# Optimization experiments

Hardware: AMD Instinct MI355X
Metric: run time of the kernel (lower is better)

The kernel has to match this reference:

```python
import jax, jax.numpy as jnp
import numpy as np

N0, N1, N2 = 80000, 40000, 20000
E1, E2 = 500000, 250000
FIN = 128        # in_channels
H = 2            # heads
C1 = 64          # hidden_channels -> layer1 out per head (concat -> 128)
C2 = 64          # out_channels -> layer2 out per head (mean over heads)
ED = 10          # edge_dim per embedding, total edge feat = 2*ED = 20
NTYPE, NTS = 23, 1158


def setup_inputs() -> dict:
    key = jax.random.key(0)
    ks = jax.random.split(key, 48)
    sc = 0.05
    inp = {
        "x": jax.random.normal(ks[0], (N0, FIN), jnp.float32),
        "ei1_src": jax.random.randint(ks[1], (E1,), 0, N0),
        "ei1_dst": jax.random.randint(ks[2], (E1,), 0, N1),
        "et1": jax.random.randint(ks[3], (E1,), 0, NTYPE),
        "ets1": jax.random.randint(ks[4], (E1,), 0, NTS),
        "ei2_src": jax.random.randint(ks[5], (E2,), 0, N1),
        "ei2_dst": jax.random.randint(ks[6], (E2,), 0, N2),
        "et2": jax.random.randint(ks[7], (E2,), 0, NTYPE),
        "ets2": jax.random.randint(ks[8], (E2,), 0, NTS),
        # shared edge embeddings (Linear(23,10), Linear(1158,10))
        "edge_W": jax.random.normal(ks[9], (ED, NTYPE), jnp.float32) * sc,
        "edge_b": jax.random.normal(ks[10], (ED,), jnp.float32) * sc,
        "time_W": jax.random.normal(ks[11], (ED, NTS), jnp.float32) * sc,
        "time_b": jax.random.normal(ks[12], (ED,), jnp.float32) * sc,
    }
    # layer 1: in=128, heads=2, C=64, concat=True (out dim 128)
    hc1 = H * C1
    inp["Wq1"] = jax.random.normal(ks[13], (hc1, FIN), jnp.float32) * sc
    inp["bq1"] = jnp.zeros((hc1,), jnp.float32)
    inp["Wk1"] = jax.random.normal(ks[14], (hc1, FIN), jnp.float32) * sc
    inp["bk1"] = jnp.zeros((hc1,), jnp.float32)
    inp["Wv1"] = jax.random.normal(ks[15], (hc1, FIN), jnp.float32) * sc
    inp["bv1"] = jnp.zeros((hc1,), jnp.float32)
    inp["We1"] = jax.random.normal(ks[16], (hc1, 2 * ED), jnp.float32) * sc
    inp["Wskip1"] = jax.random.normal(ks[17], (hc1, FIN), jnp.float32) * sc
    inp["bskip1"] = jnp.zeros((hc1,), jnp.float32)
    inp["Wbeta1"] = jax.random.normal(ks[18], (1, 3 * hc1), jnp.float32) * sc
    inp["ln_g"] = jnp.ones((hc1,), jnp.float32)
    inp["ln_b"] = jnp.zeros((hc1,), jnp.float32)
    # layer 2: in=128, heads=2, C=64, concat=False (out dim 64)
    hc2 = H * C2
    inp["Wq2"] = jax.random.normal(ks[19], (hc2, hc1), jnp.float32) * sc
    inp["bq2"] = jnp.zeros((hc2,), jnp.float32)
    inp["Wk2"] = jax.random.normal(ks[20], (hc2, hc1), jnp.float32) * sc
    inp["bk2"] = jnp.zeros((hc2,), jnp.float32)
    inp["Wv2"] = jax.random.normal(ks[21], (hc2, hc1), jnp.float32) * sc
    inp["bv2"] = jnp.zeros((hc2,), jnp.float32)
    inp["We2"] = jax.random.normal(ks[22], (hc2, 2 * ED), jnp.float32) * sc
    inp["Wskip2"] = jax.random.normal(ks[23], (C2, hc1), jnp.float32) * sc
    inp["bskip2"] = jnp.zeros((C2,), jnp.float32)
    inp["Wbeta2"] = jax.random.normal(ks[24], (1, 3 * C2), jnp.float32) * sc
    return inp


def _edge_feat(et, ets, edge_W, edge_b, time_W, time_b):
    # one_hot(e) @ W.T + b == W.T[e] + b (avoids materializing huge one-hot)
    return jnp.concatenate([jnp.take(edge_W.T, et, axis=0) + edge_b,
                            jnp.take(time_W.T, ets, axis=0) + time_b], axis=-1)


def _conv(x_src, x_dst, src, dst, ef, Wq, bq, Wk, bk, Wv, bv, We,
          Wskip, bskip, Wbeta, concat):
    n_dst = x_dst.shape[0]
    HC = Wq.shape[0]
    C = HC // H
    q = (x_dst @ Wq.T + bq).reshape(n_dst, H, C)            # [Nd,H,C]
    k = (x_src @ Wk.T + bk)[src].reshape(-1, H, C)          # [E,H,C]
    v = (x_src @ Wv.T + bv)[src].reshape(-1, H, C)
    e = (ef @ We.T).reshape(-1, H, C)
    k = k + e
    alpha = jnp.einsum('ehc,ehc->eh', q[dst], k) / np.sqrt(C).astype(np.float32)
    # segment softmax over destination nodes
    m = jax.ops.segment_max(alpha, dst, num_segments=n_dst)
    ex = jnp.exp(alpha - m[dst])
    s = jax.ops.segment_sum(ex, dst, num_segments=n_dst)
    a = ex / (s[dst] + 1e-16)                               # [E,H]
    msg = (v + e) * a[..., None]                            # [E,H,C]
    out = jax.ops.segment_sum(msg.reshape(-1, HC), dst, num_segments=n_dst)
    out = out if concat else out.reshape(n_dst, H, C).mean(axis=1)
    x_r = x_dst @ Wskip.T + bskip
    beta = jax.nn.sigmoid(
        jnp.concatenate([out, x_r, out - x_r], axis=-1) @ Wbeta.T)  # [Nd,1]
    return beta * x_r + (1.0 - beta) * out


def _layernorm(x, g, b):
    mu = x.mean(-1, keepdims=True)
    var = x.var(-1, keepdims=True)
    return (x - mu) / jnp.sqrt(var + 1e-5) * g + b


def reference(x, ei1_src, ei1_dst, et1, ets1, ei2_src, ei2_dst, et2, ets2,
              edge_W, edge_b, time_W, time_b,
              Wq1, bq1, Wk1, bk1, Wv1, bv1, We1, Wskip1, bskip1, Wbeta1,
              ln_g, ln_b,
              Wq2, bq2, Wk2, bk2, Wv2, bv2, We2, Wskip2, bskip2, Wbeta2):
    ef1 = _edge_feat(et1, ets1, edge_W, edge_b, time_W, time_b)
    h = _conv(x, x[:N1], ei1_src, ei1_dst, ef1,
              Wq1, bq1, Wk1, bk1, Wv1, bv1, We1, Wskip1, bskip1, Wbeta1,
              concat=True)
    h = jax.nn.gelu(_layernorm(h, ln_g, ln_b), approximate=False)
    ef2 = _edge_feat(et2, ets2, edge_W, edge_b, time_W, time_b)
    o = _conv(h, h[:N2], ei2_src, ei2_dst, ef2,
              Wq2, bq2, Wk2, bk2, Wv2, bv2, We2, Wskip2, bskip2, Wbeta2,
              concat=False)
    return jax.nn.log_softmax(o, axis=-1)
```

## Files before the change

### kernel.cpp

```cpp
#include <hip/hip_runtime.h>
#include <math.h>

#define N0 80000
#define N1 40000
#define N2 20000
#define E1C 500000
#define E2C 250000
#define NTYPE 23
#define NTS 1158

#define NB1 157
#define NB2 79
#define KV1B 1250
#define QR1B 625
#define CNTB 2930
#define KV2B 625
#define QR2B 313
#define FILLB 2930

#define OFF_XB    0u
#define OFF_QR1   5120000u
#define OFF_KV1   15360000u
#define OFF_H     25600000u
#define OFF_QR2   28160000u
#define OFF_KV2   32000000u
#define OFF_WB1   37120000u
#define OFF_BP1   37160000u
#define OFF_WB2   37170000u
#define OFF_BP2   37200000u
#define OFF_TA1   37210000u
#define OFF_TB1   37213000u
#define OFF_TA2   37370000u
#define OFF_TB2   37373000u
#define OFF_RP1   37530000u
#define OFF_CUR1  37580000u
#define OFF_ED1   37630000u
#define OFF_BS1   38640000u
#define OFF_RP2   38650000u
#define OFF_CUR2  38680000u
#define OFF_ED2   38710000u
#define OFF_BS2   39220000u
#define OFF_DONE  39230000u

typedef __bf16 bf16x8 __attribute__((ext_vector_type(8)));
typedef float f32x4 __attribute__((ext_vector_type(4)));

static __device__ __forceinline__ float b2f(unsigned short u) {
    union { unsigned int i; float f; } c;
    c.i = ((unsigned int)u) << 16;
    return c.f;
}
static __device__ __forceinline__ unsigned short f2b(float f) {
    unsigned int u = __float_as_uint(f);
    unsigned int r = (u + 0x7fffu + ((u >> 16) & 1u)) >> 16;
    return (unsigned short)r;
}
static __device__ __forceinline__ bf16x8 ldfrag(const unsigned short* p) {
    return *reinterpret_cast<const bf16x8*>(p);
}

template <int CTRL>
static __device__ __forceinline__ float dpp_addstep(float v) {
    int x = __builtin_amdgcn_mov_dpp(__float_as_int(v), CTRL, 0xF, 0xF, true);
    return v + __int_as_float(x);
}
static __device__ __forceinline__ float red16(float v) {
    v = dpp_addstep<0xB1>(v);
    v = dpp_addstep<0x4E>(v);
    v = dpp_addstep<0x141>(v);
    v = dpp_addstep<0x140>(v);
    return v;
}
template <int CTRL>
static __device__ __forceinline__ float dpp_maxstep(float v) {
    int x = __builtin_amdgcn_mov_dpp(__float_as_int(v), CTRL, 0xF, 0xF, true);
    return fmaxf(v, __int_as_float(x));
}
static __device__ __forceinline__ float red16max(float v) {
    v = dpp_maxstep<0xB1>(v);
    v = dpp_maxstep<0x4E>(v);
    v = dpp_maxstep<0x141>(v);
    v = dpp_maxstep<0x140>(v);
    return v;
}

#define LDSS 136

template <int NTILES>
static __device__ __forceinline__ void dev_gemm_bf16out(
    const unsigned short* __restrict__ XB, const unsigned short* __restrict__ WB,
    const float* __restrict__ BP, unsigned short* __restrict__ Y, int n, int blk,
    unsigned short* sb) {
    constexpr int COLS = NTILES * 16;
    constexpr int HALF = NTILES / 2;
    constexpr int HCOLS = HALF * 16;
    int wave = threadIdx.x >> 6, lane = threadIdx.x & 63;
    int m = lane & 15, quad = lane >> 4;
    int rowbase = blk * 64 + wave * 16;
    int arow = rowbase + m; if (arow >= n) arow = n - 1;
    unsigned short* swave = sb + wave * 16 * LDSS;
    const unsigned short* xrow = XB + (size_t)arow * 128 + quad * 8;
    bf16x8 a0 = ldfrag(xrow), a1 = ldfrag(xrow + 32);
    bf16x8 a2 = ldfrag(xrow + 64), a3 = ldfrag(xrow + 96);
    f32x4 acc[NTILES];
#pragma unroll
    for (int t = 0; t < NTILES; t++) acc[t] = (f32x4){0.f, 0.f, 0.f, 0.f};
#pragma unroll
    for (int t = 0; t < NTILES; t++) {
        const unsigned short* wt = WB + (size_t)t * 2048 + lane * 8;
        acc[t] = __builtin_amdgcn_mfma_f32_16x16x32_bf16(a0, ldfrag(wt), acc[t], 0, 0, 0);
        acc[t] = __builtin_amdgcn_mfma_f32_16x16x32_bf16(a1, ldfrag(wt + 512), acc[t], 0, 0, 0);
        acc[t] = __builtin_amdgcn_mfma_f32_16x16x32_bf16(a2, ldfrag(wt + 1024), acc[t], 0, 0, 0);
        acc[t] = __builtin_amdgcn_mfma_f32_16x16x32_bf16(a3, ldfrag(wt + 1536), acc[t], 0, 0, 0);
    }
    int tswz_bit = (quad >> 1) & 1;
#pragma unroll
    for (int half = 0; half < 2; half++) {
#pragma unroll
        for (int t = 0; t < HALF; t++) {
            int tt = half * HALF + t;
            int tsw = t ^ tswz_bit;
            float b = BP[tt * 16 + m];
#pragma unroll
            for (int r = 0; r < 4; r++)
                swave[(quad * 4 + r) * LDSS + tsw * 16 + m] = f2b(acc[tt][r] + b);
        }
#pragma unroll
        for (int i = 0; i < 4; i++) {
            int idx = i * 64 + lane;
            int r = idx / (HCOLS / 8), g = idx % (HCOLS / 8);
            int gs = g ^ (((r >> 3) & 1) << 1);
            int grow = rowbase + r;
            if (grow < n) {
                uint4 v = *(const uint4*)&swave[r * LDSS + gs * 8];
                *(uint4*)(Y + (size_t)grow * COLS + half * HCOLS + g * 8) = v;
            }
        }
    }
}

template <int NTILES>
static __device__ __forceinline__ void dev_gemm_f32out(
    const unsigned short* __restrict__ XB, const unsigned short* __restrict__ WB,
    const float* __restrict__ BP, float* __restrict__ Y, int n, int blk) {
    constexpr int COLS = NTILES * 16;
    int wave = threadIdx.x >> 6, lane = threadIdx.x & 63;
    int m = lane & 15, quad = lane >> 4;
    int rowbase = blk * 64 + wave * 16;
    int arow = rowbase + m; if (arow >= n) arow = n - 1;
    const unsigned short* xrow = XB + (size_t)arow * 128 + quad * 8;
    bf16x8 a0 = ldfrag(xrow), a1 = ldfrag(xrow + 32);
    bf16x8 a2 = ldfrag(xrow + 64), a3 = ldfrag(xrow + 96);
    f32x4 acc[NTILES];
#pragma unroll
    for (int t = 0; t < NTILES; t++) acc[t] = (f32x4){0.f, 0.f, 0.f, 0.f};
#pragma unroll
    for (int t = 0; t < NTILES; t++) {
        const unsigned short* wt = WB + (size_t)t * 2048 + lane * 8;
        acc[t] = __builtin_amdgcn_mfma_f32_16x16x32_bf16(a0, ldfrag(wt), acc[t], 0, 0, 0);
        acc[t] = __builtin_amdgcn_mfma_f32_16x16x32_bf16(a1, ldfrag(wt + 512), acc[t], 0, 0, 0);
        acc[t] = __builtin_amdgcn_mfma_f32_16x16x32_bf16(a2, ldfrag(wt + 1024), acc[t], 0, 0, 0);
        acc[t] = __builtin_amdgcn_mfma_f32_16x16x32_bf16(a3, ldfrag(wt + 1536), acc[t], 0, 0, 0);
    }
#pragma unroll
    for (int t = 0; t < NTILES; t++) {
        float b = BP[t * 16 + m];
#pragma unroll
        for (int r = 0; r < 4; r++) {
            int grow = rowbase + quad * 4 + r;
            if (grow < n) Y[(size_t)grow * COLS + t * 16 + m] = acc[t][r] + b;
        }
    }
}

__global__ __launch_bounds__(256) void prep(
    const float* __restrict__ x, unsigned short* __restrict__ XB,
    const float* __restrict__ Wk1, const float* __restrict__ Wv1,
    const float* __restrict__ Wq1, const float* __restrict__ Wskip1,
    const float* __restrict__ bk1, const float* __restrict__ bv1,
    const float* __restrict__ bq1, const float* __restrict__ bskip1,
    const float* __restrict__ Wk2, const float* __restrict__ Wv2,
    const float* __restrict__ Wq2, const float* __restrict__ Wskip2,
    const float* __restrict__ bk2, const float* __restrict__ bv2,
    const float* __restrict__ bq2, const float* __restrict__ bskip2,
    unsigned short* __restrict__ WB1, float* __restrict__ BP1,
    unsigned short* __restrict__ WB2, float* __restrict__ BP2,
    const float* __restrict__ edge_W, const float* __restrict__ edge_b,
    const float* __restrict__ time_W, const float* __restrict__ time_b,
    const float* __restrict__ We1, const float* __restrict__ We2,
    float* __restrict__ TA1, float* __restrict__ TB1,
    float* __restrict__ TA2, float* __restrict__ TB2,
    int* __restrict__ cnt1, int* __restrict__ cnt2, int* __restrict__ done) {
    int tid = blockIdx.x * blockDim.x + threadIdx.x;
    int stride = gridDim.x * blockDim.x;
    for (int i = tid; i < N0 * 32; i += stride) {
        float4 v = *(const float4*)(x + (size_t)i * 4);
        ushort4 u;
        u.x = f2b(v.x); u.y = f2b(v.y); u.z = f2b(v.z); u.w = f2b(v.w);
        *(ushort4*)(XB + (size_t)i * 4) = u;
    }
    for (int i = tid; i < 512 * 128; i += stride) {
        int j = i & 7, l = (i >> 3) & 63, ks = (i >> 9) & 3, t = i >> 11;
        int row = t * 16 + (l & 15);
        int col = ks * 32 + ((l >> 4) & 3) * 8 + j;
        const float* w; int off;
        if (row < 128) { w = Wk1; off = 0; }
        else if (row < 256) { w = Wv1; off = 128; }
        else if (row < 384) { w = Wq1; off = 256; }
        else { w = Wskip1; off = 384; }
        WB1[i] = f2b(w[(size_t)(row - off) * 128 + col]);
    }
    for (int i = tid; i < 512; i += stride) {
        const float* b; int off;
        if (i < 128) { b = bk1; off = 0; }
        else if (i < 256) { b = bv1; off = 128; }
        else if (i < 384) { b = bq1; off = 256; }
        else { b = bskip1; off = 384; }
        BP1[i] = b[i - off];
    }
    for (int i = tid; i < 448 * 128; i += stride) {
        int j = i & 7, l = (i >> 3) & 63, ks = (i >> 9) & 3, t = i >> 11;
        int row = t * 16 + (l & 15);
        int col = ks * 32 + ((l >> 4) & 3) * 8 + j;
        const float* w; int off;
        if (row < 128) { w = Wk2; off = 0; }
        else if (row < 256) { w = Wv2; off = 128; }
        else if (row < 384) { w = Wq2; off = 256; }
        else { w = Wskip2; off = 384; }
        WB2[i] = f2b(w[(size_t)(row - off) * 128 + col]);
    }
    for (int i = tid; i < 448; i += stride) {
        const float* b; int off;
        if (i < 128) { b = bk2; off = 0; }
        else if (i < 256) { b = bv2; off = 128; }
        else if (i < 384) { b = bq2; off = 256; }
        else { b = bskip2; off = 384; }
        BP2[i] = b[i - off];
    }
    const int TBL = (NTYPE + NTS) * 128;
    for (int i = tid; i < TBL; i += stride) {
        if (i < NTYPE * 128) {
            int e = i >> 7, c = i & 127;
            float s1 = 0.f, s2 = 0.f;
#pragma unroll
            for (int j = 0; j < 10; j++) {
                float fj = edge_W[j * NTYPE + e] + edge_b[j];
                s1 += fj * We1[c * 20 + j];
                s2 += fj * We2[c * 20 + j];
            }
            TA1[i] = s1; TA2[i] = s2;
        } else {
            int u = i - NTYPE * 128;
            int ts = u >> 7, c = u & 127;
            float s1 = 0.f, s2 = 0.f;
#pragma unroll
            for (int j = 0; j < 10; j++) {
                float fj = time_W[j * NTS + ts] + time_b[j];
                s1 += fj * We1[c * 20 + 10 + j];
                s2 += fj * We2[c * 20 + 10 + j];
            }
            TB1[u] = s1; TB2[u] = s2;
        }
    }
    for (int i = tid; i < N1 + N2 + 2; i += stride) {
        if (i < N1) cnt1[i] = 0;
        else if (i < N1 + N2) cnt2[i - N1] = 0;
        else done[i - N1 - N2] = 0;
    }
}

__global__ __launch_bounds__(256) void mega_l1(
    const unsigned short* __restrict__ XB,
    const unsigned short* __restrict__ WB1, const float* __restrict__ BP1,
    unsigned short* __restrict__ KV1, float* __restrict__ QR1,
    const int* __restrict__ d1, const int* __restrict__ d2,
    int* __restrict__ cnt1, int* __restrict__ cnt2) {
    __shared__ unsigned short sbuf[4 * 16 * LDSS];
    int b = blockIdx.x;
    if (b < KV1B) {
        dev_gemm_bf16out<16>(XB, WB1, BP1, KV1, N0, b, sbuf);
    } else if (b < KV1B + QR1B) {
        dev_gemm_f32out<16>(XB, WB1 + 256 * 128, BP1 + 256, QR1, N1, b - KV1B);
    } else {
        int t = (b - KV1B - QR1B) * 256 + threadIdx.x;
        if (t < E1C) atomicAdd(&cnt1[d1[t]], 1);
        else {
            t -= E1C;
            if (t < E2C) atomicAdd(&cnt2[d2[t]], 1);
        }
    }
}

__global__ __launch_bounds__(256) void gemm_l2(
    const unsigned short* __restrict__ H,
    const unsigned short* __restrict__ WB2, const float* __restrict__ BP2,
    unsigned short* __restrict__ KV2, float* __restrict__ QR2) {
    __shared__ unsigned short sbuf[4 * 16 * LDSS];
    int b = blockIdx.x;
    if (b < KV2B) dev_gemm_bf16out<16>(H, WB2, BP2, KV2, N1, b, sbuf);
    else dev_gemm_f32out<12>(H, WB2 + 256 * 128, BP2 + 256, QR2, N2, b - KV2B);
}

__global__ __launch_bounds__(256) void csr_scan(
    int* __restrict__ cnt1, int* __restrict__ bs1, int* __restrict__ rp1,
    int* __restrict__ cnt2, int* __restrict__ bs2, int* __restrict__ rp2,
    int* __restrict__ done) {
    __shared__ int s[256];
    __shared__ int amlast;
    int b = blockIdx.x;
    int* cnt; int* bs; int* rp; int n, lb;
    if (b < NB1) { cnt = cnt1; bs = bs1; rp = rp1; n = N1; lb = b; }
    else { cnt = cnt2; bs = bs2; rp = rp2; n = N2; lb = b - NB1; }
    int t = lb * 256 + threadIdx.x;
    int v = (t < n) ? cnt[t] : 0;
    s[threadIdx.x] = v;
    __syncthreads();
    for (int off = 128; off; off >>= 1) {
        if (threadIdx.x < off) s[threadIdx.x] += s[threadIdx.x + off];
        __syncthreads();
    }
    if (threadIdx.x == 0) {
        atomicExch(&bs[lb], s[0]);
        __threadfence();
        int prev = atomicAdd(&done[0], 1);
        amlast = (prev == NB1 + NB2 - 1) ? 1 : 0;
    }
    __syncthreads();
    if (amlast) {
        int tt = threadIdx.x;
        int v1 = (tt < NB1) ? atomicAdd(&bs1[tt], 0) : 0;
        s[tt] = v1;
        __syncthreads();
        for (int off = 1; off < 256; off <<= 1) {
            int u = (tt >= off) ? s[tt - off] : 0;
            __syncthreads();
            s[tt] += u;
            __syncthreads();
        }
        if (tt < NB1) atomicExch(&bs1[tt], s[tt] - v1);
        __syncthreads();
        int v2 = (tt < NB2) ? atomicAdd(&bs2[tt], 0) : 0;
        s[tt] = v2;
        __syncthreads();
        for (int off = 1; off < 256; off <<= 1) {
            int u = (tt >= off) ? s[tt - off] : 0;
            __syncthreads();
            s[tt] += u;
            __syncthreads();
        }
        if (tt < NB2) atomicExch(&bs2[tt], s[tt] - v2);
        __threadfence();
        __syncthreads();
        if (tt == 0) atomicExch(&done[1], 1);
    }
    if (threadIdx.x == 0) {
        while (atomicAdd(&done[1], 0) == 0) __builtin_amdgcn_s_sleep(1);
    }
    __syncthreads();
    __threadfence();
    int base = atomicAdd(&bs[lb], 0);
    s[threadIdx.x] = v;
    __syncthreads();
    for (int off = 1; off < 256; off <<= 1) {
        int u = (threadIdx.x >= off) ? s[threadIdx.x - off] : 0;
        __syncthreads();
        s[threadIdx.x] += u;
        __syncthreads();
    }
    int incl = s[threadIdx.x];
    if (t < n) { rp[t] = base + incl - v; cnt[t] = 0; }
    if (t == n - 1) rp[n] = base + incl;
}

__global__ __launch_bounds__(256) void fill_both(
    const int* __restrict__ d1, const int* __restrict__ s1,
    const int* __restrict__ et1, const int* __restrict__ ets1,
    const int* __restrict__ rp1, int* __restrict__ cur1, uint2* __restrict__ ed1,
    const int* __restrict__ d2, const int* __restrict__ s2,
    const int* __restrict__ et2, const int* __restrict__ ets2,
    const int* __restrict__ rp2, int* __restrict__ cur2, uint2* __restrict__ ed2) {
    int t = blockIdx.x * 256 + threadIdx.x;
    if (t < E1C) {
        int d = d1[t];
        int pos = rp1[d] + atomicAdd(&cur1[d], 1);
        ed1[pos] = make_uint2((unsigned)s1[t],
                              (unsigned)(et1[t] | (ets1[t] << 16)));
    } else {
        t -= E1C;
        if (t < E2C) {
            int d = d2[t];
            int pos = rp2[d] + atomicAdd(&cur2[d], 1);
            ed2[pos] = make_uint2((unsigned)s2[t],
                                  (unsigned)(et2[t] | (ets2[t] << 16)));
        }
    }
}

__global__ __launch_bounds__(256) void agg_layer1(
    const int* __restrict__ rowptr, const uint2* __restrict__ ED,
    const float* __restrict__ TA, const float* __restrict__ TB,
    const float* __restrict__ QR, const unsigned short* __restrict__ KV,
    const float* __restrict__ Wbeta,
    const float* __restrict__ ln_g, const float* __restrict__ ln_b,
    unsigned short* __restrict__ hout, int n) {
    int wid = (blockIdx.x * blockDim.x + threadIdx.x) >> 6;
    int lane = threadIdx.x & 63;
    if (wid >= n) return;
    int s = lane >> 5, cg = lane & 15;
    int co = ((lane >> 4) & 1) * 64 + 4 * cg;
    int beg = rowptr[wid], end = rowptr[wid + 1];
    float4 q4 = *(const float4*)(QR + (size_t)wid * 256 + co);
    float ax = 0.f, ay = 0.f, az = 0.f, aw = 0.f, suma = 0.f;
    int p = beg + s;
    if (p < end) {
        uint2 d0 = ED[p];
        int p1 = p + 2;
        bool m1 = p1 < end;
        uint2 dn = ED[m1 ? p1 : beg];
        int sn0 = (int)d0.x, t0 = (int)(d0.y & 0xFFFF), ts0 = (int)(d0.y >> 16);
        float4 ta0 = *(const float4*)(TA + t0 * 128 + co);
        float4 tb0 = *(const float4*)(TB + ts0 * 128 + co);
        const unsigned short* kv0 = KV + (size_t)sn0 * 256;
        ushort4 ku0 = *(const ushort4*)(kv0 + co);
        ushort4 vu0 = *(const ushort4*)(kv0 + 128 + co);
        for (;;) {
            int p2 = p1 + 2;
            bool m2 = p2 < end;
            uint2 dnn = ED[m2 ? p2 : beg];
            int sn1 = (int)dn.x, t1 = (int)(dn.y & 0xFFFF), ts1 = (int)(dn.y >> 16);
            float4 ta1 = *(const float4*)(TA + t1 * 128 + co);
            float4 tb1 = *(const float4*)(TB + ts1 * 128 + co);
            const unsigned short* kv1 = KV + (size_t)sn1 * 256;
            ushort4 ku1 = *(const ushort4*)(kv1 + co);
            ushort4 vu1 = *(const ushort4*)(kv1 + 128 + co);
            float e0c = ta0.x + tb0.x, e1c = ta0.y + tb0.y;
            float e2c = ta0.z + tb0.z, e3c = ta0.w + tb0.w;
            float pp = q4.x * (b2f(ku0.x) + e0c) + q4.y * (b2f(ku0.y) + e1c)
                     + q4.z * (b2f(ku0.z) + e2c) + q4.w * (b2f(ku0.w) + e3c);
            pp = red16(pp);
            float a = __expf(pp * 0.125f);
            ax += a * (b2f(vu0.x) + e0c); ay += a * (b2f(vu0.y) + e1c);
            az += a * (b2f(vu0.z) + e2c); aw += a * (b2f(vu0.w) + e3c);
            suma += a;
            if (!m1) break;
            p1 = p2; m1 = m2; dn = dnn;
            ta0 = ta1; tb0 = tb1; ku0 = ku1; vu0 = vu1;
        }
    }
    ax += __shfl_xor(ax, 32); ay += __shfl_xor(ay, 32);
    az += __shfl_xor(az, 32); aw += __shfl_xor(aw, 32);
    suma += __shfl_xor(suma, 32);
    float inv_s = 1.f / (suma + 1e-16f);
    float ox = ax * inv_s, oy = ay * inv_s, oz = az * inv_s, ow = aw * inv_s;
    float4 r4 = *(const float4*)(QR + (size_t)wid * 256 + 128 + co);
    float4 wo = *(const float4*)(Wbeta + co);
    float4 wr = *(const float4*)(Wbeta + 128 + co);
    float4 wd = *(const float4*)(Wbeta + 256 + co);
    float pb = wo.x * ox + wr.x * r4.x + wd.x * (ox - r4.x)
             + wo.y * oy + wr.y * r4.y + wd.y * (oy - r4.y)
             + wo.z * oz + wr.z * r4.z + wd.z * (oz - r4.z)
             + wo.w * ow + wr.w * r4.w + wd.w * (ow - r4.w);
    pb = red16(pb);
    pb += __shfl_xor(pb, 16);
    float beta = 1.f / (1.f + __expf(-pb));
    float gx = beta * r4.x + (1.f - beta) * ox;
    float gy = beta * r4.y + (1.f - beta) * oy;
    float gz = beta * r4.z + (1.f - beta) * oz;
    float gw = beta * r4.w + (1.f - beta) * ow;
    float sm = gx + gy + gz + gw;
    float sq = gx * gx + gy * gy + gz * gz + gw * gw;
    sm = red16(sm); sm += __shfl_xor(sm, 16);
    sq = red16(sq); sq += __shfl_xor(sq, 16);
    float mu = sm * (1.f / 128.f);
    float var = sq * (1.f / 128.f) - mu * mu;
    float inv = rsqrtf(var + 1e-5f);
    float4 lg = *(const float4*)(ln_g + co);
    float4 lb = *(const float4*)(ln_b + co);
    float yx = (gx - mu) * inv * lg.x + lb.x;
    float yy = (gy - mu) * inv * lg.y + lb.y;
    float yz = (gz - mu) * inv * lg.z + lb.z;
    float yw = (gw - mu) * inv * lg.w + lb.w;
    const float ISQ2 = 0.70710678118654752f;
    yx = 0.5f * yx * (1.f + erff(yx * ISQ2));
    yy = 0.5f * yy * (1.f + erff(yy * ISQ2));
    yz = 0.5f * yz * (1.f + erff(yz * ISQ2));
    yw = 0.5f * yw * (1.f + erff(yw * ISQ2));
    if (s == 0) {
        ushort4 hv;
        hv.x = f2b(yx); hv.y = f2b(yy); hv.z = f2b(yz); hv.w = f2b(yw);
        *(ushort4*)(hout + (size_t)wid * 128 + co) = hv;
    }
}

__global__ __launch_bounds__(256) void agg_layer2(
    const int* __restrict__ rowptr, const uint2* __restrict__ ED,
    const float* __restrict__ TA, const float* __restrict__ TB,
    const float* __restrict__ QR, const unsigned short* __restrict__ KV,
    const float* __restrict__ Wbeta,
    float* __restrict__ o, int n) {
    int wid = (blockIdx.x * blockDim.x + threadIdx.x) >> 6;
    int lane = threadIdx.x & 63;
    if (wid >= n) return;
    int s = lane >> 5, cg = lane & 15;
    int co = ((lane >> 4) & 1) * 64 + 4 * cg;
    int beg = rowptr[wid], end = rowptr[wid + 1];
    float4 q4 = *(const float4*)(QR + (size_t)wid * 192 + co);
    float ax = 0.f, ay = 0.f, az = 0.f, aw = 0.f, suma = 0.f;
    int p = beg + s;
    if (p < end) {
        uint2 d0 = ED[p];
        int p1 = p + 2;
        bool m1 = p1 < end;
        uint2 dn = ED[m1 ? p1 : beg];
        int sn0 = (int)d0.x, t0 = (int)(d0.y & 0xFFFF), ts0 = (int)(d0.y >> 16);
        float4 ta0 = *(const float4*)(TA + t0 * 128 + co);
        float4 tb0 = *(const float4*)(TB + ts0 * 128 + co);
        const unsigned short* kv0 = KV + (size_t)sn0 * 256;
        ushort4 ku0 = *(const ushort4*)(kv0 + co);
        ushort4 vu0 = *(const ushort4*)(kv0 + 128 + co);
        for (;;) {
            int p2 = p1 + 2;
            bool m2 = p2 < end;
            uint2 dnn = ED[m2 ? p2 : beg];
            int sn1 = (int)dn.x, t1 = (int)(dn.y & 0xFFFF), ts1 = (int)(dn.y >> 16);
            float4 ta1 = *(const float4*)(TA + t1 * 128 + co);
            float4 tb1 = *(const float4*)(TB + ts1 * 128 + co);
            const unsigned short* kv1 = KV + (size_t)sn1 * 256;
            ushort4 ku1 = *(const ushort4*)(kv1 + co);
            ushort4 vu1 = *(const ushort4*)(kv1 + 128 + co);
            float e0c = ta0.x + tb0.x, e1c = ta0.y + tb0.y;
            float e2c = ta0.z + tb0.z, e3c = ta0.w + tb0.w;
            float pp = q4.x * (b2f(ku0.x) + e0c) + q4.y * (b2f(ku0.y) + e1c)
                     + q4.z * (b2f(ku0.z) + e2c) + q4.w * (b2f(ku0.w) + e3c);
            pp = red16(pp);
            float a = __expf(pp * 0.125f);
            ax += a * (b2f(vu0.x) + e0c); ay += a * (b2f(vu0.y) + e1c);
            az += a * (b2f(vu0.z) + e2c); aw += a * (b2f(vu0.w) + e3c);
            suma += a;
            if (!m1) break;
            p1 = p2; m1 = m2; dn = dnn;
            ta0 = ta1; tb0 = tb1; ku0 = ku1; vu0 = vu1;
        }
    }
    ax += __shfl_xor(ax, 32); ay += __shfl_xor(ay, 32);
    az += __shfl_xor(az, 32); aw += __shfl_xor(aw, 32);
    suma += __shfl_xor(suma, 32);
    float inv_s = 1.f / (suma + 1e-16f);
    float ox = ax * inv_s, oy = ay * inv_s, oz = az * inv_s, ow = aw * inv_s;
    ox = 0.5f * (ox + __shfl_xor(ox, 16));
    oy = 0.5f * (oy + __shfl_xor(oy, 16));
    oz = 0.5f * (oz + __shfl_xor(oz, 16));
    ow = 0.5f * (ow + __shfl_xor(ow, 16));
    float4 r4 = *(const float4*)(QR + (size_t)wid * 192 + 128 + 4 * cg);
    float4 wo = *(const float4*)(Wbeta + 4 * cg);
    float4 wr = *(const float4*)(Wbeta + 64 + 4 * cg);
    float4 wd = *(const float4*)(Wbeta + 128 + 4 * cg);
    float pb = wo.x * ox + wr.x * r4.x + wd.x * (ox - r4.x)
             + wo.y * oy + wr.y * r4.y + wd.y * (oy - r4.y)
             + wo.z * oz + wr.z * r4.z + wd.z * (oz - r4.z)
             + wo.w * ow + wr.w * r4.w + wd.w * (ow - r4.w);
    pb = red16(pb);
    float beta = 1.f / (1.f + __expf(-pb));
    float vx = beta * r4.x + (1.f - beta) * ox;
    float vy = beta * r4.y + (1.f - beta) * oy;
    float vz = beta * r4.z + (1.f - beta) * oz;
    float vw = beta * r4.w + (1.f - beta) * ow;
    float m = fmaxf(fmaxf(vx, vy), fmaxf(vz, vw));
    m = red16max(m);
    float se = __expf(vx - m) + __expf(vy - m) + __expf(vz - m) + __expf(vw - m);
    se = red16(se);
    float lse = m + logf(se);
    if (lane < 16)
        *(float4*)(o + (size_t)wid * 64 + 4 * cg) =
            make_float4(vx - lse, vy - lse, vz - lse, vw - lse);
}

extern "C" void kernel_launch(void* const* d_in, const int* in_sizes, int n_in,
                              void* d_out, int out_size, void* d_ws, size_t ws_size,
                              hipStream_t stream) {
    const float* x        = (const float*)d_in[0];
    const int*   ei1_src  = (const int*)d_in[1];
    const int*   ei1_dst  = (const int*)d_in[2];
    const int*   et1      = (const int*)d_in[3];
    const int*   ets1     = (const int*)d_in[4];
    const int*   ei2_src  = (const int*)d_in[5];
    const int*   ei2_dst  = (const int*)d_in[6];
    const int*   et2      = (const int*)d_in[7];
    const int*   ets2     = (const int*)d_in[8];
    const float* edge_W   = (const float*)d_in[9];
    const float* edge_b   = (const float*)d_in[10];
    const float* time_W   = (const float*)d_in[11];
    const float* time_b   = (const float*)d_in[12];
    const float* Wq1      = (const float*)d_in[13];
    const float* bq1      = (const float*)d_in[14];
    const float* Wk1      = (const float*)d_in[15];
    const float* bk1      = (const float*)d_in[16];
    const float* Wv1      = (const float*)d_in[17];
    const float* bv1      = (const float*)d_in[18];
    const float* We1      = (const float*)d_in[19];
    const float* Wskip1   = (const float*)d_in[20];
    const float* bskip1   = (const float*)d_in[21];
    const float* Wbeta1   = (const float*)d_in[22];
    const float* ln_g     = (const float*)d_in[23];
    const float* ln_b     = (const float*)d_in[24];
    const float* Wq2      = (const float*)d_in[25];
    const float* bq2      = (const float*)d_in[26];
    const float* Wk2      = (const float*)d_in[27];
    const float* bk2      = (const float*)d_in[28];
    const float* Wv2      = (const float*)d_in[29];
    const float* bv2      = (const float*)d_in[30];
    const float* We2      = (const float*)d_in[31];
    const float* Wskip2   = (const float*)d_in[32];
    const float* bskip2   = (const float*)d_in[33];
    const float* Wbeta2   = (const float*)d_in[34];

    float* ws = (float*)d_ws;
    unsigned short* xb  = (unsigned short*)(ws + OFF_XB);
    float* qr1          = ws + OFF_QR1;
    unsigned short* kv1 = (unsigned short*)(ws + OFF_KV1);
    unsigned short* h   = (unsigned short*)(ws + OFF_H);
    float* qr2          = ws + OFF_QR2;
    unsigned short* kv2 = (unsigned short*)(ws + OFF_KV2);
    unsigned short* wb1 = (unsigned short*)(ws + OFF_WB1);
    float* bp1          = ws + OFF_BP1;
    unsigned short* wb2 = (unsigned short*)(ws + OFF_WB2);
    float* bp2          = ws + OFF_BP2;
    float* ta1          = ws + OFF_TA1;
    float* tb1          = ws + OFF_TB1;
    float* ta2          = ws + OFF_TA2;
    float* tb2          = ws + OFF_TB2;
    int*   rp1          = (int*)(ws + OFF_RP1);
    int*   cur1         = (int*)(ws + OFF_CUR1);
    uint2* ed1          = (uint2*)(ws + OFF_ED1);
    int*   bs1          = (int*)(ws + OFF_BS1);
    int*   rp2          = (int*)(ws + OFF_RP2);
    int*   cur2         = (int*)(ws + OFF_CUR2);
    uint2* ed2          = (uint2*)(ws + OFF_ED2);
    int*   bs2          = (int*)(ws + OFF_BS2);
    int*   done         = (int*)(ws + OFF_DONE);

    prep<<<2048, 256, 0, stream>>>(
        x, xb,
        Wk1, Wv1, Wq1, Wskip1, bk1, bv1, bq1, bskip1,
        Wk2, Wv2, Wq2, Wskip2, bk2, bv2, bq2, bskip2,
        wb1, bp1, wb2, bp2,
        edge_W, edge_b, time_W, time_b, We1, We2,
        ta1, tb1, ta2, tb2, cur1, cur2, done);
    mega_l1<<<KV1B + QR1B + CNTB, 256, 0, stream>>>(
        xb, wb1, bp1, kv1, qr1, ei1_dst, ei2_dst, cur1, cur2);
    csr_scan<<<NB1 + NB2, 256, 0, stream>>>(cur1, bs1, rp1, cur2, bs2, rp2, done);
    fill_both<<<FILLB, 256, 0, stream>>>(
        ei1_dst, ei1_src, et1, ets1, rp1, cur1, ed1,
        ei2_dst, ei2_src, et2, ets2, rp2, cur2, ed2);
    agg_layer1<<<(N1 + 3) / 4, 256, 0, stream>>>(rp1, ed1,
        ta1, tb1, qr1, kv1, Wbeta1, ln_g, ln_b, h, N1);
    gemm_l2<<<KV2B + QR2B, 256, 0, stream>>>(h, wb2, bp2, kv2, qr2);
    agg_layer2<<<(N2 + 3) / 4, 256, 0, stream>>>(rp2, ed2,
        ta2, tb2, qr2, kv2, Wbeta2, (float*)d_out, N2);
}
```

Before: 392.4 us.

## Use persistent atomic-ticket scheduling and deeper prefetch in aggregation kernels

Both aggregation kernels become persistent. Each wave grabs batches of four destination nodes from a global atomic ticket counter instead of being assigned one node per wave, and the grid shrinks to a fixed block count. The edge loop now prefetches two edges ahead instead of one, to hide more gather latency. The atomic ticket balances the uneven per-node degree, at the cost of atomic contention and more live registers.

```diff
diff --git a/kernel.cpp b/kernel.cpp
--- a/kernel.cpp
+++ b/kernel.cpp
@@ -262,7 +262,7 @@
             TB1[u] = s1; TB2[u] = s2;
         }
     }
-    for (int i = tid; i < N1 + N2 + 2; i += stride) {
+    for (int i = tid; i < N1 + N2 + 4; i += stride) {
         if (i < N1) cnt1[i] = 0;
         else if (i < N1 + N2) cnt2[i - N1] = 0;
         else done[i - N1 - N2] = 0;
@@ -402,93 +402,108 @@
     const float* __restrict__ QR, const unsigned short* __restrict__ KV,
     const float* __restrict__ Wbeta,
     const float* __restrict__ ln_g, const float* __restrict__ ln_b,
-    unsigned short* __restrict__ hout, int n) {
-    int wid = (blockIdx.x * blockDim.x + threadIdx.x) >> 6;
+    unsigned short* __restrict__ hout, int n, int* __restrict__ ticket) {
     int lane = threadIdx.x & 63;
-    if (wid >= n) return;
     int s = lane >> 5, cg = lane & 15;
     int co = ((lane >> 4) & 1) * 64 + 4 * cg;
-    int beg = rowptr[wid], end = rowptr[wid + 1];
-    float4 q4 = *(const float4*)(QR + (size_t)wid * 256 + co);
-    float ax = 0.f, ay = 0.f, az = 0.f, aw = 0.f, suma = 0.f;
-    int p = beg + s;
-    if (p < end) {
-        uint2 d0 = ED[p];
-        int p1 = p + 2;
-        bool m1 = p1 < end;
-        uint2 dn = ED[m1 ? p1 : beg];
-        int sn0 = (int)d0.x, t0 = (int)(d0.y & 0xFFFF), ts0 = (int)(d0.y >> 16);
-        float4 ta0 = *(const float4*)(TA + t0 * 128 + co);
-        float4 tb0 = *(const float4*)(TB + ts0 * 128 + co);
-        const unsigned short* kv0 = KV + (size_t)sn0 * 256;
-        ushort4 ku0 = *(const ushort4*)(kv0 + co);
-        ushort4 vu0 = *(const ushort4*)(kv0 + 128 + co);
-        for (;;) {
-            int p2 = p1 + 2;
-            bool m2 = p2 < end;
-            uint2 dnn = ED[m2 ? p2 : beg];
-            int sn1 = (int)dn.x, t1 = (int)(dn.y & 0xFFFF), ts1 = (int)(dn.y >> 16);
-            float4 ta1 = *(const float4*)(TA + t1 * 128 + co);
-            float4 tb1 = *(const float4*)(TB + ts1 * 128 + co);
-            const unsigned short* kv1 = KV + (size_t)sn1 * 256;
-            ushort4 ku1 = *(const ushort4*)(kv1 + co);
-            ushort4 vu1 = *(const ushort4*)(kv1 + 128 + co);
-            float e0c = ta0.x + tb0.x, e1c = ta0.y + tb0.y;
-            float e2c = ta0.z + tb0.z, e3c = ta0.w + tb0.w;
-            float pp = q4.x * (b2f(ku0.x) + e0c) + q4.y * (b2f(ku0.y) + e1c)
-                     + q4.z * (b2f(ku0.z) + e2c) + q4.w * (b2f(ku0.w) + e3c);
-            pp = red16(pp);
-            float a = __expf(pp * 0.125f);
-            ax += a * (b2f(vu0.x) + e0c); ay += a * (b2f(vu0.y) + e1c);
-            az += a * (b2f(vu0.z) + e2c); aw += a * (b2f(vu0.w) + e3c);
-            suma += a;
-            if (!m1) break;
-            p1 = p2; m1 = m2; dn = dnn;
-            ta0 = ta1; tb0 = tb1; ku0 = ku1; vu0 = vu1;
-        }
-    }
-    ax += __shfl_xor(ax, 32); ay += __shfl_xor(ay, 32);
-    az += __shfl_xor(az, 32); aw += __shfl_xor(aw, 32);
-    suma += __shfl_xor(suma, 32);
-    float inv_s = 1.f / (suma + 1e-16f);
-    float ox = ax * inv_s, oy = ay * inv_s, oz = az * inv_s, ow = aw * inv_s;
-    float4 r4 = *(const float4*)(QR + (size_t)wid * 256 + 128 + co);
-    float4 wo = *(const float4*)(Wbeta + co);
-    float4 wr = *(const float4*)(Wbeta + 128 + co);
-    float4 wd = *(const float4*)(Wbeta + 256 + co);
-    float pb = wo.x * ox + wr.x * r4.x + wd.x * (ox - r4.x)
-             + wo.y * oy + wr.y * r4.y + wd.y * (oy - r4.y)
-             + wo.z * oz + wr.z * r4.z + wd.z * (oz - r4.z)
-             + wo.w * ow + wr.w * r4.w + wd.w * (ow - r4.w);
-    pb = red16(pb);
-    pb += __shfl_xor(pb, 16);
-    float beta = 1.f / (1.f + __expf(-pb));
-    float gx = beta * r4.x + (1.f - beta) * ox;
-    float gy = beta * r4.y + (1.f - beta) * oy;
-    float gz = beta * r4.z + (1.f - beta) * oz;
-    float gw = beta * r4.w + (1.f - beta) * ow;
-    float sm = gx + gy + gz + gw;
-    float sq = gx * gx + gy * gy + gz * gz + gw * gw;
-    sm = red16(sm); sm += __shfl_xor(sm, 16);
-    sq = red16(sq); sq += __shfl_xor(sq, 16);
-    float mu = sm * (1.f / 128.f);
-    float var = sq * (1.f / 128.f) - mu * mu;
-    float inv = rsqrtf(var + 1e-5f);
-    float4 lg = *(const float4*)(ln_g + co);
-    float4 lb = *(const float4*)(ln_b + co);
-    float yx = (gx - mu) * inv * lg.x + lb.x;
-    float yy = (gy - mu) * inv * lg.y + lb.y;
-    float yz = (gz - mu) * inv * lg.z + lb.z;
-    float yw = (gw - mu) * inv * lg.w + lb.w;
-    const float ISQ2 = 0.70710678118654752f;
-    yx = 0.5f * yx * (1.f + erff(yx * ISQ2));
-    yy = 0.5f * yy * (1.f + erff(yy * ISQ2));
-    yz = 0.5f * yz * (1.f + erff(yz * ISQ2));
-    yw = 0.5f * yw * (1.f + erff(yw * ISQ2));
-    if (s == 0) {
-        ushort4 hv;
-        hv.x = f2b(yx); hv.y = f2b(yy); hv.z = f2b(yz); hv.w = f2b(yw);
-        *(ushort4*)(hout + (size_t)wid * 128 + co) = hv;
+    for (;;) {
+        int base0 = 0;
+        if (lane == 0) base0 = atomicAdd(ticket, 4);
+        int nb = __shfl(base0, 0);
+        if (nb >= n) return;
+        int lim = nb + 4 < n ? nb + 4 : n;
+        for (int wid = nb; wid < lim; wid++) {
+            int beg = rowptr[wid], end = rowptr[wid + 1];
+            float4 q4 = *(const float4*)(QR + (size_t)wid * 256 + co);
+            float ax = 0.f, ay = 0.f, az = 0.f, aw = 0.f, suma = 0.f;
+            int p = beg + s;
+            if (p < end) {
+                uint2 d0 = ED[p];
+                int pA = p + 2;  bool mA = pA < end;
+                uint2 d1 = ED[mA ? pA : beg];
+                int pB = p + 4;  bool mB = pB < end;
+                uint2 d2 = ED[mB ? pB : beg];
+                int sn0 = (int)d0.x, t0 = (int)(d0.y & 0xFFFF), ts0 = (int)(d0.y >> 16);
+                float4 ta0 = *(const float4*)(TA + t0 * 128 + co);
+                float4 tb0 = *(const float4*)(TB + ts0 * 128 + co);
+                const unsigned short* kv0 = KV + (size_t)sn0 * 256;
+                ushort4 ku0 = *(const ushort4*)(kv0 + co);
+                ushort4 vu0 = *(const ushort4*)(kv0 + 128 + co);
+                int sn1 = (int)d1.x, t1 = (int)(d1.y & 0xFFFF), ts1 = (int)(d1.y >> 16);
+                float4 ta1 = *(const float4*)(TA + t1 * 128 + co);
+                float4 tb1 = *(const float4*)(TB + ts1 * 128 + co);
+                const unsigned short* kv1 = KV + (size_t)sn1 * 256;
+                ushort4 ku1 = *(const ushort4*)(kv1 + co);
+                ushort4 vu1 = *(const ushort4*)(kv1 + 128 + co);
+                for (;;) {
+                    int pC = pB + 2; bool mC = pC < end;
+                    uint2 d3 = ED[mC ? pC : beg];
+                    int sn2 = (int)d2.x, t2 = (int)(d2.y & 0xFFFF), ts2 = (int)(d2.y >> 16);
+                    float4 ta2 = *(const float4*)(TA + t2 * 128 + co);
+                    float4 tb2 = *(const float4*)(TB + ts2 * 128 + co);
+                    const unsigned short* kv2 = KV + (size_t)sn2 * 256;
+                    ushort4 ku2 = *(const ushort4*)(kv2 + co);
+                    ushort4 vu2 = *(const ushort4*)(kv2 + 128 + co);
+                    float e0c = ta0.x + tb0.x, e1c = ta0.y + tb0.y;
+                    float e2c = ta0.z + tb0.z, e3c = ta0.w + tb0.w;
+                    float pp = q4.x * (b2f(ku0.x) + e0c) + q4.y * (b2f(ku0.y) + e1c)
+                             + q4.z * (b2f(ku0.z) + e2c) + q4.w * (b2f(ku0.w) + e3c);
+                    pp = red16(pp);
+                    float a = __expf(pp * 0.125f);
+                    ax += a * (b2f(vu0.x) + e0c); ay += a * (b2f(vu0.y) + e1c);
+                    az += a * (b2f(vu0.z) + e2c); aw += a * (b2f(vu0.w) + e3c);
+                    suma += a;
+                    if (!mA) break;
+                    ta0 = ta1; tb0 = tb1; ku0 = ku1; vu0 = vu1;
+                    ta1 = ta2; tb1 = tb2; ku1 = ku2; vu1 = vu2;
+                    d2 = d3;
+                    mA = mB; mB = mC; pB = pC;
+                }
+            }
+            ax += __shfl_xor(ax, 32); ay += __shfl_xor(ay, 32);
+            az += __shfl_xor(az, 32); aw += __shfl_xor(aw, 32);
+            suma += __shfl_xor(suma, 32);
+            float inv_s = 1.f / (suma + 1e-16f);
+            float ox = ax * inv_s, oy = ay * inv_s, oz = az * inv_s, ow = aw * inv_s;
+            float4 r4 = *(const float4*)(QR + (size_t)wid * 256 + 128 + co);
+            float4 wo = *(const float4*)(Wbeta + co);
+            float4 wr = *(const float4*)(Wbeta + 128 + co);
+            float4 wd = *(const float4*)(Wbeta + 256 + co);
+            float pb = wo.x * ox + wr.x * r4.x + wd.x * (ox - r4.x)
+                     + wo.y * oy + wr.y * r4.y + wd.y * (oy - r4.y)
+                     + wo.z * oz + wr.z * r4.z + wd.z * (oz - r4.z)
+                     + wo.w * ow + wr.w * r4.w + wd.w * (ow - r4.w);
+            pb = red16(pb);
+            pb += __shfl_xor(pb, 16);
+            float beta = 1.f / (1.f + __expf(-pb));
+            float gx = beta * r4.x + (1.f - beta) * ox;
+            float gy = beta * r4.y + (1.f - beta) * oy;
+            float gz = beta * r4.z + (1.f - beta) * oz;
+            float gw = beta * r4.w + (1.f - beta) * ow;
+            float sm = gx + gy + gz + gw;
+            float sq = gx * gx + gy * gy + gz * gz + gw * gw;
+            sm = red16(sm); sm += __shfl_xor(sm, 16);
+            sq = red16(sq); sq += __shfl_xor(sq, 16);
+            float mu = sm * (1.f / 128.f);
+            float var = sq * (1.f / 128.f) - mu * mu;
+            float inv = rsqrtf(var + 1e-5f);
+            float4 lg = *(const float4*)(ln_g + co);
+            float4 lb = *(const float4*)(ln_b + co);
+            float yx = (gx - mu) * inv * lg.x + lb.x;
+            float yy = (gy - mu) * inv * lg.y + lb.y;
+            float yz = (gz - mu) * inv * lg.z + lb.z;
+            float yw = (gw - mu) * inv * lg.w + lb.w;
+            const float ISQ2 = 0.70710678118654752f;
+            yx = 0.5f * yx * (1.f + erff(yx * ISQ2));
+            yy = 0.5f * yy * (1.f + erff(yy * ISQ2));
+            yz = 0.5f * yz * (1.f + erff(yz * ISQ2));
+            yw = 0.5f * yw * (1.f + erff(yw * ISQ2));
+            if (s == 0) {
+                ushort4 hv;
+                hv.x = f2b(yx); hv.y = f2b(yy); hv.z = f2b(yz); hv.w = f2b(yw);
+                *(ushort4*)(hout + (size_t)wid * 128 + co) = hv;
+            }
+        }
     }
 }
 
@@ -497,82 +512,97 @@
     const float* __restrict__ TA, const float* __restrict__ TB,
     const float* __restrict__ QR, const unsigned short* __restrict__ KV,
     const float* __restrict__ Wbeta,
-    float* __restrict__ o, int n) {
-    int wid = (blockIdx.x * blockDim.x + threadIdx.x) >> 6;
+    float* __restrict__ o, int n, int* __restrict__ ticket) {
     int lane = threadIdx.x & 63;
-    if (wid >= n) return;
     int s = lane >> 5, cg = lane & 15;
     int co = ((lane >> 4) & 1) * 64 + 4 * cg;
-    int beg = rowptr[wid], end = rowptr[wid + 1];
-    float4 q4 = *(const float4*)(QR + (size_t)wid * 192 + co);
-    float ax = 0.f, ay = 0.f, az = 0.f, aw = 0.f, suma = 0.f;
-    int p = beg + s;
-    if (p < end) {
-        uint2 d0 = ED[p];
-        int p1 = p + 2;
-        bool m1 = p1 < end;
-        uint2 dn = ED[m1 ? p1 : beg];
-        int sn0 = (int)d0.x, t0 = (int)(d0.y & 0xFFFF), ts0 = (int)(d0.y >> 16);
-        float4 ta0 = *(const float4*)(TA + t0 * 128 + co);
-        float4 tb0 = *(const float4*)(TB + ts0 * 128 + co);
-        const unsigned short* kv0 = KV + (size_t)sn0 * 256;
-        ushort4 ku0 = *(const ushort4*)(kv0 + co);
-        ushort4 vu0 = *(const ushort4*)(kv0 + 128 + co);
-        for (;;) {
-            int p2 = p1 + 2;
-            bool m2 = p2 < end;
-            uint2 dnn = ED[m2 ? p2 : beg];
-            int sn1 = (int)dn.x, t1 = (int)(dn.y & 0xFFFF), ts1 = (int)(dn.y >> 16);
-            float4 ta1 = *(const float4*)(TA + t1 * 128 + co);
-            float4 tb1 = *(const float4*)(TB + ts1 * 128 + co);
-            const unsigned short* kv1 = KV + (size_t)sn1 * 256;
-            ushort4 ku1 = *(const ushort4*)(kv1 + co);
-            ushort4 vu1 = *(const ushort4*)(kv1 + 128 + co);
-            float e0c = ta0.x + tb0.x, e1c = ta0.y + tb0.y;
-            float e2c = ta0.z + tb0.z, e3c = ta0.w + tb0.w;
-            float pp = q4.x * (b2f(ku0.x) + e0c) + q4.y * (b2f(ku0.y) + e1c)
-                     + q4.z * (b2f(ku0.z) + e2c) + q4.w * (b2f(ku0.w) + e3c);
-            pp = red16(pp);
-            float a = __expf(pp * 0.125f);
-            ax += a * (b2f(vu0.x) + e0c); ay += a * (b2f(vu0.y) + e1c);
-            az += a * (b2f(vu0.z) + e2c); aw += a * (b2f(vu0.w) + e3c);
-            suma += a;
-            if (!m1) break;
-            p1 = p2; m1 = m2; dn = dnn;
-            ta0 = ta1; tb0 = tb1; ku0 = ku1; vu0 = vu1;
-        }
-    }
-    ax += __shfl_xor(ax, 32); ay += __shfl_xor(ay, 32);
-    az += __shfl_xor(az, 32); aw += __shfl_xor(aw, 32);
-    suma += __shfl_xor(suma, 32);
-    float inv_s = 1.f / (suma + 1e-16f);
-    float ox = ax * inv_s, oy = ay * inv_s, oz = az * inv_s, ow = aw * inv_s;
-    ox = 0.5f * (ox + __shfl_xor(ox, 16));
-    oy = 0.5f * (oy + __shfl_xor(oy, 16));
-    oz = 0.5f * (oz + __shfl_xor(oz, 16));
-    ow = 0.5f * (ow + __shfl_xor(ow, 16));
-    float4 r4 = *(const float4*)(QR + (size_t)wid * 192 + 128 + 4 * cg);
-    float4 wo = *(const float4*)(Wbeta + 4 * cg);
-    float4 wr = *(const float4*)(Wbeta + 64 + 4 * cg);
-    float4 wd = *(const float4*)(Wbeta + 128 + 4 * cg);
-    float pb = wo.x * ox + wr.x * r4.x + wd.x * (ox - r4.x)
-             + wo.y * oy + wr.y * r4.y + wd.y * (oy - r4.y)
-             + wo.z * oz + wr.z * r4.z + wd.z * (oz - r4.z)
-             + wo.w * ow + wr.w * r4.w + wd.w * (ow - r4.w);
-    pb = red16(pb);
-    float beta = 1.f / (1.f + __expf(-pb));
-    float vx = beta * r4.x + (1.f - beta) * ox;
-    float vy = beta * r4.y + (1.f - beta) * oy;
-    float vz = beta * r4.z + (1.f - beta) * oz;
-    float vw = beta * r4.w + (1.f - beta) * ow;
-    float m = fmaxf(fmaxf(vx, vy), fmaxf(vz, vw));
-    m = red16max(m);
-    float se = __expf(vx - m) + __expf(vy - m) + __expf(vz - m) + __expf(vw - m);
-    se = red16(se);
-    float lse = m + logf(se);
-    if (lane < 16)
-        *(float4*)(o + (size_t)wid * 64 + 4 * cg) =
-            make_float4(vx - lse, vy - lse, vz - lse, vw - lse);
+    for (;;) {
+        int base0 = 0;
+        if (lane == 0) base0 = atomicAdd(ticket, 4);
+        int nb = __shfl(base0, 0);
+        if (nb >= n) return;
+        int lim = nb + 4 < n ? nb + 4 : n;
+        for (int wid = nb; wid < lim; wid++) {
+            int beg = rowptr[wid], end = rowptr[wid + 1];
+            float4 q4 = *(const float4*)(QR + (size_t)wid * 192 + co);
+            float ax = 0.f, ay = 0.f, az = 0.f, aw = 0.f, suma = 0.f;
+            int p = beg + s;
+            if (p < end) {
+                uint2 d0 = ED[p];
+                int pA = p + 2;  bool mA = pA < end;
+                uint2 d1 = ED[mA ? pA : beg];
+                int pB = p + 4;  bool mB = pB < end;
+                uint2 d2 = ED[mB ? pB : beg];
+                int sn0 = (int)d0.x, t0 = (int)(d0.y & 0xFFFF), ts0 = (int)(d0.y >> 16);
+                float4 ta0 = *(const float4*)(TA + t0 * 128 + co);
+                float4 tb0 = *(const float4*)(TB + ts0 * 128 + co);
+                const unsigned short* kv0 = KV + (size_t)sn0 * 256;
+                ushort4 ku0 = *(const ushort4*)(kv0 + co);
+                ushort4 vu0 = *(const ushort4*)(kv0 + 128 + co);
+                int sn1 = (int)d1.x, t1 = (int)(d1.y & 0xFFFF), ts1 = (int)(d1.y >> 16);
+                float4 ta1 = *(const float4*)(TA + t1 * 128 + co);
+                float4 tb1 = *(const float4*)(TB + ts1 * 128 + co);
+                const unsigned short* kv1 = KV + (size_t)sn1 * 256;
+                ushort4 ku1 = *(const ushort4*)(kv1 + co);
+                ushort4 vu1 = *(const ushort4*)(kv1 + 128 + co);
+                for (;;) {
+                    int pC = pB + 2; bool mC = pC < end;
+                    uint2 d3 = ED[mC ? pC : beg];
+                    int sn2 = (int)d2.x, t2 = (int)(d2.y & 0xFFFF), ts2 = (int)(d2.y >> 16);
+                    float4 ta2 = *(const float4*)(TA + t2 * 128 + co);
+                    float4 tb2 = *(const float4*)(TB + ts2 * 128 + co);
+                    const unsigned short* kv2 = KV + (size_t)sn2 * 256;
+                    ushort4 ku2 = *(const ushort4*)(kv2 + co);
+                    ushort4 vu2 = *(const ushort4*)(kv2 + 128 + co);
+                    float e0c = ta0.x + tb0.x, e1c = ta0.y + tb0.y;
+                    float e2c = ta0.z + tb0.z, e3c = ta0.w + tb0.w;
+                    float pp = q4.x * (b2f(ku0.x) + e0c) + q4.y * (b2f(ku0.y) + e1c)
+                             + q4.z * (b2f(ku0.z) + e2c) + q4.w * (b2f(ku0.w) + e3c);
+                    pp = red16(pp);
+                    float a = __expf(pp * 0.125f);
+                    ax += a * (b2f(vu0.x) + e0c); ay += a * (b2f(vu0.y) + e1c);
+                    az += a * (b2f(vu0.z) + e2c); aw += a * (b2f(vu0.w) + e3c);
+                    suma += a;
+                    if (!mA) break;
+                    ta0 = ta1; tb0 = tb1; ku0 = ku1; vu0 = vu1;
+                    ta1 = ta2; tb1 = tb2; ku1 = ku2; vu1 = vu2;
+                    d2 = d3;
+                    mA = mB; mB = mC; pB = pC;
+                }
+            }
+            ax += __shfl_xor(ax, 32); ay += __shfl_xor(ay, 32);
+            az += __shfl_xor(az, 32); aw += __shfl_xor(aw, 32);
+            suma += __shfl_xor(suma, 32);
+            float inv_s = 1.f / (suma + 1e-16f);
+            float ox = ax * inv_s, oy = ay * inv_s, oz = az * inv_s, ow = aw * inv_s;
+            ox = 0.5f * (ox + __shfl_xor(ox, 16));
+            oy = 0.5f * (oy + __shfl_xor(oy, 16));
+            oz = 0.5f * (oz + __shfl_xor(oz, 16));
+            ow = 0.5f * (ow + __shfl_xor(ow, 16));
+            float4 r4 = *(const float4*)(QR + (size_t)wid * 192 + 128 + 4 * cg);
+            float4 wo = *(const float4*)(Wbeta + 4 * cg);
+            float4 wr = *(const float4*)(Wbeta + 64 + 4 * cg);
+            float4 wd = *(const float4*)(Wbeta + 128 + 4 * cg);
+            float pb = wo.x * ox + wr.x * r4.x + wd.x * (ox - r4.x)
+                     + wo.y * oy + wr.y * r4.y + wd.y * (oy - r4.y)
+                     + wo.z * oz + wr.z * r4.z + wd.z * (oz - r4.z)
+                     + wo.w * ow + wr.w * r4.w + wd.w * (ow - r4.w);
+            pb = red16(pb);
+            float beta = 1.f / (1.f + __expf(-pb));
+            float vx = beta * r4.x + (1.f - beta) * ox;
+            float vy = beta * r4.y + (1.f - beta) * oy;
+            float vz = beta * r4.z + (1.f - beta) * oz;
+            float vw = beta * r4.w + (1.f - beta) * ow;
+            float m = fmaxf(fmaxf(vx, vy), fmaxf(vz, vw));
+            m = red16max(m);
+            float se = __expf(vx - m) + __expf(vy - m) + __expf(vz - m) + __expf(vw - m);
+            se = red16(se);
+            float lse = m + logf(se);
+            if (lane < 16)
+                *(float4*)(o + (size_t)wid * 64 + 4 * cg) =
+                    make_float4(vx - lse, vy - lse, vz - lse, vw - lse);
+        }
+    }
 }
 
 extern "C" void kernel_launch(void* const* d_in, const int* in_sizes, int n_in,
@@ -652,9 +682,9 @@
     fill_both<<<FILLB, 256, 0, stream>>>(
         ei1_dst, ei1_src, et1, ets1, rp1, cur1, ed1,
         ei2_dst, ei2_src, et2, ets2, rp2, cur2, ed2);
-    agg_layer1<<<(N1 + 3) / 4, 256, 0, stream>>>(rp1, ed1,
-        ta1, tb1, qr1, kv1, Wbeta1, ln_g, ln_b, h, N1);
+    agg_layer1<<<1024, 256, 0, stream>>>(rp1, ed1,
+        ta1, tb1, qr1, kv1, Wbeta1, ln_g, ln_b, h, N1, done + 2);
     gemm_l2<<<KV2B + QR2B, 256, 0, stream>>>(h, wb2, bp2, kv2, qr2);
-    agg_layer2<<<(N2 + 3) / 4, 256, 0, stream>>>(rp2, ed2,
-        ta2, tb2, qr2, kv2, Wbeta2, (float*)d_out, N2);
-}
+    agg_layer2<<<512, 256, 0, stream>>>(rp2, ed2,
+        ta2, tb2, qr2, kv2, Wbeta2, (float*)d_out, N2, done + 3);
+}
```

Result: slower. 592.8 us (+51.1%).
